# Performance work log

Hardware: AMD Instinct MI355X
Metric: run time of the kernel (lower is better)

Reference implementation:

```python
import jax, jax.numpy as jnp
import numpy as np

V, D, L = 128, 512, 4
B, S = 64, 1024
H = 2 * D          # LSTM hidden size
G = 4 * H          # gate dim (i,f,g,o)
RMS_EPS = 1.1920929e-07  # torch.finfo(float32).eps (nn.RMSNorm default eps=None)
LN_EPS = 1e-5


def setup_inputs() -> dict:
    key = jax.random.key(0)
    ks = jax.random.split(key, 8)
    sc = 1.0 / np.sqrt(H).astype(np.float32)
    return {
        "tokens": jax.random.randint(ks[0], (B, S), 0, V),
        "embedding": jax.random.normal(ks[1], (V, D), jnp.float32) * 0.02,
        "pre_norm_w": jnp.ones((L, D), jnp.float32),
        "W_ih": jax.random.normal(ks[2], (L, G, D), jnp.float32) * sc,
        "W_hh": jax.random.normal(ks[3], (L, G, H), jnp.float32) * sc,
        "b_ih": jnp.zeros((L, G), jnp.float32),
        "b_hh": jnp.zeros((L, G), jnp.float32),
        "W_out": jax.random.normal(ks[4], (L, D, H), jnp.float32) * sc,
        "b_out": jnp.zeros((L, D), jnp.float32),
        "ln_w": jnp.ones((L, D), jnp.float32),
        "ln_b": jnp.zeros((L, D), jnp.float32),
        "final_norm_w": jnp.ones((D,), jnp.float32),
        "head_W": jax.random.normal(ks[5], (V, D), jnp.float32) / np.sqrt(D),
        "head_b": jnp.zeros((V,), jnp.float32),
    }


def rmsnorm(x, w):
    var = jnp.mean(x * x, axis=-1, keepdims=True)
    return x * jax.lax.rsqrt(var + RMS_EPS) * w


def layernorm(x, w, b):
    mu = jnp.mean(x, axis=-1, keepdims=True)
    var = jnp.mean(jnp.square(x - mu), axis=-1, keepdims=True)
    return (x - mu) * jax.lax.rsqrt(var + LN_EPS) * w + b


def lstm(x, W_ih, W_hh, b_ih, b_hh):
    # x: [B,S,D] -> precompute input gates [S,B,4H], scan over time
    xg = jnp.einsum('bsd,gd->sbg', x, W_ih) + b_ih + b_hh
    bsz = x.shape[0]
    hdim = W_hh.shape[1]

    def step(carry, gx):
        h, c = carry
        g = gx + h @ W_hh.T
        i, f, gg, o = jnp.split(g, 4, axis=-1)
        c = jax.nn.sigmoid(f) * c + jax.nn.sigmoid(i) * jnp.tanh(gg)
        h = jax.nn.sigmoid(o) * jnp.tanh(c)
        return (h, c), h

    init = (jnp.zeros((bsz, hdim), x.dtype), jnp.zeros((bsz, hdim), x.dtype))
    _, hs = jax.lax.scan(step, init, xg)
    return hs.transpose(1, 0, 2)  # [B,S,H]


def reference(tokens, embedding, pre_norm_w, W_ih, W_hh, b_ih, b_hh,
              W_out, b_out, ln_w, ln_b, final_norm_w, head_W, head_b):
    x = embedding[tokens]  # [B,S,D]
    n_layers = pre_norm_w.shape[0]
    for l in range(n_layers):
        nx = rmsnorm(x, pre_norm_w[l])
        h = lstm(nx, W_ih[l], W_hh[l], b_ih[l], b_hh[l])
        out = jnp.einsum('bsh,dh->bsd', h, W_out[l]) + b_out[l]
        x = x + layernorm(out + nx, ln_w[l], ln_b[l])
    x = rmsnorm(x, final_norm_w)
    last = x[:, -1, :]                 # last token; dropout is identity (eval)
    return last @ head_W.T + head_b    # [B,V]
```

## Files before the change

kernel.cpp:

```cpp
#include <hip/hip_runtime.h>
#include <stdint.h>

typedef short bf16x8 __attribute__((ext_vector_type(8)));
typedef short s16x4  __attribute__((ext_vector_type(4)));
typedef float f32x4  __attribute__((ext_vector_type(4)));

__device__ __forceinline__ short f2bf(float f) {
  unsigned u = __builtin_bit_cast(unsigned, f);
  unsigned r = (u + 0x7fffu + ((u >> 16) & 1u)) >> 16;
  return (short)r;
}
__device__ __forceinline__ float bf2f(short s) {
  unsigned u = ((unsigned)(unsigned short)s) << 16;
  return __builtin_bit_cast(float, u);
}
__device__ __forceinline__ float sigf(float x) { return 1.f / (1.f + __expf(-x)); }
__device__ __forceinline__ float tanhf_(float x) {
  float e = __expf(2.f * x);
  return 1.f - 2.f / (e + 1.f);
}
__device__ __forceinline__ float wave_sum(float v) {
#pragma unroll
  for (int o = 32; o; o >>= 1) v += __shfl_xor(v, o, 64);
  return v;
}

__global__ void cvt_k(const float* __restrict__ a, short* __restrict__ o, int n) {
  int i = (blockIdx.x * 256 + threadIdx.x) * 4;
  if (i >= n) return;
  float4 v = *(const float4*)(a + i);
  s16x4 r;
  r[0] = f2bf(v.x); r[1] = f2bf(v.y); r[2] = f2bf(v.z); r[3] = f2bf(v.w);
  *(s16x4*)(o + i) = r;
}

__global__ void embed_k(const int* __restrict__ toks, const float* __restrict__ emb,
                        short* __restrict__ x) {
  const int t = blockIdx.x;
  const int tok = toks[t];
  const float4* src = (const float4*)(emb + (size_t)tok * 512);
  float4 a = src[threadIdx.x * 2], b = src[threadIdx.x * 2 + 1];
  bf16x8 o;
  o[0] = f2bf(a.x); o[1] = f2bf(a.y); o[2] = f2bf(a.z); o[3] = f2bf(a.w);
  o[4] = f2bf(b.x); o[5] = f2bf(b.y); o[6] = f2bf(b.z); o[7] = f2bf(b.w);
  *(bf16x8*)(x + (size_t)t * 512 + threadIdx.x * 8) = o;
}

__global__ void rms_k(const short* __restrict__ x, const float* __restrict__ w,
                      short* __restrict__ nx, int s0, int chsh, int chm) {
  const int t = blockIdx.x, b = t >> chsh, sl = t & chm;
  const short* xr = x + ((size_t)b * 1024 + s0 + sl) * 512;
  const int d0 = threadIdx.x * 8;
  bf16x8 xv = *(const bf16x8*)(xr + d0);
  float f[8];
  float ss = 0.f;
#pragma unroll
  for (int i = 0; i < 8; ++i) { f[i] = bf2f(xv[i]); ss += f[i] * f[i]; }
  ss = wave_sum(ss);
  float rs = rsqrtf(ss * (1.f / 512.f) + 1.1920929e-07f);
  float4 w0 = *(const float4*)(w + d0), w1 = *(const float4*)(w + d0 + 4);
  bf16x8 o;
  o[0] = f2bf(f[0] * rs * w0.x); o[1] = f2bf(f[1] * rs * w0.y);
  o[2] = f2bf(f[2] * rs * w0.z); o[3] = f2bf(f[3] * rs * w0.w);
  o[4] = f2bf(f[4] * rs * w1.x); o[5] = f2bf(f[5] * rs * w1.y);
  o[6] = f2bf(f[6] * rs * w1.z); o[7] = f2bf(f[7] * rs * w1.w);
  *(bf16x8*)(nx + (size_t)t * 512 + d0) = o;
}

template <int KD, int MODE>
__global__ __launch_bounds__(256, 2) void gemm_bt_k(
    const short* __restrict__ A, const short* __restrict__ Bw, short* __restrict__ Cb,
    const float* __restrict__ bias0, const float* __restrict__ bias1, int chsh, int chm) {
  __shared__ __align__(16) short lA[128 * 64];
  __shared__ __align__(16) short lB[128 * 64];
  const int tid = threadIdx.x, lane = tid & 63, wv = tid >> 6;
  const int wm = wv >> 1, wn = wv & 1;
  const int tm = blockIdx.x, tn = blockIdx.y;
  f32x4 acc[4][4] = {};
  const short* Abase = A + (size_t)tm * 128 * KD;
  const short* Bbase = Bw + (size_t)tn * 128 * KD;
  for (int k0 = 0; k0 < KD; k0 += 64) {
    __syncthreads();
#pragma unroll
    for (int i = 0; i < 4; ++i) {
      int e = i * 2048 + tid * 8;
      int row = e >> 6, c8 = (e >> 3) & 7;
      int dsto = row * 64 + ((c8 ^ (row & 7)) << 3);
      *(bf16x8*)(lA + dsto) = *(const bf16x8*)(Abase + (size_t)row * KD + k0 + (c8 << 3));
      *(bf16x8*)(lB + dsto) = *(const bf16x8*)(Bbase + (size_t)row * KD + k0 + (c8 << 3));
    }
    __syncthreads();
#pragma unroll
    for (int kk = 0; kk < 2; ++kk) {
      bf16x8 af[4], bfr[4];
#pragma unroll
      for (int i = 0; i < 4; ++i) {
        int ra = wm * 64 + i * 16 + (lane & 15);
        int rb = wn * 64 + i * 16 + (lane & 15);
        int k8 = kk * 4 + (lane >> 4);
        af[i] = *(const bf16x8*)(lA + ra * 64 + ((k8 ^ (ra & 7)) << 3));
        bfr[i] = *(const bf16x8*)(lB + rb * 64 + ((k8 ^ (rb & 7)) << 3));
      }
#pragma unroll
      for (int i = 0; i < 4; ++i)
#pragma unroll
        for (int j = 0; j < 4; ++j)
          acc[i][j] = __builtin_amdgcn_mfma_f32_16x16x32_bf16(af[i], bfr[j], acc[i][j], 0, 0, 0);
    }
  }
#pragma unroll
  for (int i = 0; i < 4; ++i) {
    int rbase = tm * 128 + wm * 64 + i * 16 + (lane >> 4) * 4;
#pragma unroll
    for (int j = 0; j < 4; ++j) {
      int col = tn * 128 + wn * 64 + j * 16 + (lane & 15);
      float badd = 0.f;
      if constexpr (MODE == 0) badd = bias0[col] + bias1[col];
#pragma unroll
      for (int r = 0; r < 4; ++r) {
        int rowi = rbase + r;
        float v = acc[i][j][r] + badd;
        if constexpr (MODE == 0) {
          int b = rowi >> chsh, sl = rowi & chm;
          size_t off = (size_t)sl * 262144 + (size_t)((col >> 4) & 63) * 4096 +
                       (size_t)(b >> 4) * 1024 + (size_t)(col >> 10) * 256 +
                       (size_t)(b & 15) * 16 + (size_t)(col & 15);
          Cb[off] = f2bf(v);
        } else {
          Cb[(size_t)rowi * 512 + col] = f2bf(v);
        }
      }
    }
  }
}

__global__ __launch_bounds__(256, 1) void lstm_rec_k(
    const short* __restrict__ xg,
    short* __restrict__ h_all,
    const short* __restrict__ Whh,
    short* __restrict__ ring,
    float* __restrict__ c_st,
    int CH, int chsh) {
  const int tid = threadIdx.x, lane = tid & 63, wq = tid >> 6;
  const int grp = blockIdx.x >> 6, w = blockIdx.x & 63;
  const int j0 = w * 16, b0 = grp * 16;
  __shared__ __align__(16) short hstg[16384];
  __shared__ float gates[4][16][16];
  bf16x8 wf[32];
  {
    const short* wrow = Whh + (size_t)(wq * 1024 + j0 + (lane & 15)) * 1024 + (lane >> 4) * 8;
#pragma unroll
    for (int kt = 0; kt < 32; ++kt) wf[kt] = *(const bf16x8*)(wrow + kt * 32);
  }
  const int bb = tid >> 3, jj = (tid & 7) * 2;
  float c0 = 0.f, c1 = 0.f;
  if (tid < 128) {
    c0 = c_st[(size_t)(b0 + bb) * 1024 + j0 + jj];
    c1 = c_st[(size_t)(b0 + bb) * 1024 + j0 + jj + 1];
  }
  const short* xgl = xg + (size_t)(w * 4 + grp) * 1024 + wq * 256 +
                     (size_t)(lane & 15) * 16 + (lane >> 4) * 4;
  s16x4 cur = *(const s16x4*)xgl;

  for (int s = 0; s < CH; ++s) {
    const short* slot = ring + (size_t)s * 65536;
    unsigned long long hl0[8], hl1[8];
    unsigned mask = 0;
    while (mask != 0xFFFFu) {
#pragma unroll
      for (int it = 0; it < 8; ++it) {
        int si = it * 256 + tid;
        int kt = si >> 6, sl = si & 63;
        const short* gp = slot + (size_t)(b0 + (sl & 15)) * 1024 + kt * 32 + (sl >> 4) * 8;
        if (!(mask & (1u << (2 * it))))
          hl0[it] = __hip_atomic_load((const unsigned long long*)gp, __ATOMIC_RELAXED,
                                      __HIP_MEMORY_SCOPE_AGENT);
        if (!(mask & (1u << (2 * it + 1))))
          hl1[it] = __hip_atomic_load((const unsigned long long*)(gp + 4), __ATOMIC_RELAXED,
                                      __HIP_MEMORY_SCOPE_AGENT);
      }
      unsigned m = 0;
#pragma unroll
      for (int it = 0; it < 8; ++it) {
        unsigned ok0 = (((unsigned)hl0[it] != 0x7F7F7F7Fu) &
                        ((unsigned)(hl0[it] >> 32) != 0x7F7F7F7Fu)) ? 1u : 0u;
        unsigned ok1 = (((unsigned)hl1[it] != 0x7F7F7F7Fu) &
                        ((unsigned)(hl1[it] >> 32) != 0x7F7F7F7Fu)) ? 1u : 0u;
        m |= (ok0 << (2 * it)) | (ok1 << (2 * it + 1));
      }
      mask = m;
      if (mask != 0xFFFFu) __builtin_amdgcn_s_sleep(1);
    }
#pragma unroll
    for (int it = 0; it < 8; ++it) {
      int si = it * 256 + tid;
      unsigned long long* dst = (unsigned long long*)hstg + (size_t)si * 2;
      dst[0] = hl0[it]; dst[1] = hl1[it];
    }
    __syncthreads();
    f32x4 a0, a1 = {0.f, 0.f, 0.f, 0.f}, a2 = {0.f, 0.f, 0.f, 0.f}, a3 = {0.f, 0.f, 0.f, 0.f};
#pragma unroll
    for (int r = 0; r < 4; ++r) a0[r] = bf2f(cur[r]);
    if (s + 1 < CH) cur = *(const s16x4*)(xgl + (size_t)(s + 1) * 262144);
#pragma unroll
    for (int kt = 0; kt < 32; kt += 4) {
      a0 = __builtin_amdgcn_mfma_f32_16x16x32_bf16(
          wf[kt], *(const bf16x8*)(hstg + kt * 512 + lane * 8), a0, 0, 0, 0);
      a1 = __builtin_amdgcn_mfma_f32_16x16x32_bf16(
          wf[kt + 1], *(const bf16x8*)(hstg + (kt + 1) * 512 + lane * 8), a1, 0, 0, 0);
      a2 = __builtin_amdgcn_mfma_f32_16x16x32_bf16(
          wf[kt + 2], *(const bf16x8*)(hstg + (kt + 2) * 512 + lane * 8), a2, 0, 0, 0);
      a3 = __builtin_amdgcn_mfma_f32_16x16x32_bf16(
          wf[kt + 3], *(const bf16x8*)(hstg + (kt + 3) * 512 + lane * 8), a3, 0, 0, 0);
    }
    f32x4 acc = (a0 + a1) + (a2 + a3);
#pragma unroll
    for (int r = 0; r < 4; ++r) gates[wq][lane & 15][(lane >> 4) * 4 + r] = acc[r];
    __syncthreads();
    if (tid < 128) {
      float i0 = gates[0][bb][jj], i1 = gates[0][bb][jj + 1];
      float f0 = gates[1][bb][jj], f1 = gates[1][bb][jj + 1];
      float g0 = gates[2][bb][jj], g1 = gates[2][bb][jj + 1];
      float o0 = gates[3][bb][jj], o1 = gates[3][bb][jj + 1];
      c0 = sigf(f0) * c0 + sigf(i0) * tanhf_(g0);
      c1 = sigf(f1) * c1 + sigf(i1) * tanhf_(g1);
      float h0 = sigf(o0) * tanhf_(c0);
      float h1 = sigf(o1) * tanhf_(c1);
      unsigned pk = (unsigned)(unsigned short)f2bf(h0) |
                    (((unsigned)(unsigned short)f2bf(h1)) << 16);
      __hip_atomic_store(
          (unsigned*)(ring + (size_t)(s + 1) * 65536 + (size_t)(b0 + bb) * 1024 + j0 + jj),
          pk, __ATOMIC_RELAXED, __HIP_MEMORY_SCOPE_AGENT);
      *(unsigned*)(h_all + ((size_t)(((b0 + bb) << chsh) + s)) * 1024 + j0 + jj) = pk;
    }
  }
  if (tid < 128) {
    c_st[(size_t)(b0 + bb) * 1024 + j0 + jj] = c0;
    c_st[(size_t)(b0 + bb) * 1024 + j0 + jj + 1] = c1;
  }
}

__global__ void ln_k(short* __restrict__ x, const short* __restrict__ outc,
                     const short* __restrict__ nxc, const float* __restrict__ bout,
                     const float* __restrict__ lnw, const float* __restrict__ lnb,
                     int s0, int chsh, int chm) {
  const int t = blockIdx.x, b = t >> chsh, sl = t & chm;
  short* xr = x + ((size_t)b * 1024 + s0 + sl) * 512;
  const int d0 = threadIdx.x * 8;
  bf16x8 ov = *(const bf16x8*)(outc + (size_t)t * 512 + d0);
  bf16x8 nv = *(const bf16x8*)(nxc + (size_t)t * 512 + d0);
  float v[8];
  float s = 0.f, ss = 0.f;
#pragma unroll
  for (int i = 0; i < 8; ++i) {
    v[i] = bf2f(ov[i]) + bout[d0 + i] + bf2f(nv[i]);
    s += v[i]; ss += v[i] * v[i];
  }
  s = wave_sum(s); ss = wave_sum(ss);
  float mu = s * (1.f / 512.f);
  float var = ss * (1.f / 512.f) - mu * mu;
  float rsd = rsqrtf(var + 1e-5f);
  bf16x8 xv = *(const bf16x8*)(xr + d0);
  bf16x8 o;
#pragma unroll
  for (int i = 0; i < 8; ++i)
    o[i] = f2bf(bf2f(xv[i]) + (v[i] - mu) * rsd * lnw[d0 + i] + lnb[d0 + i]);
  *(bf16x8*)(xr + d0) = o;
}

__global__ void head_k(const short* __restrict__ x, const float* __restrict__ fw,
                       const float* __restrict__ hW, const float* __restrict__ hb,
                       float* __restrict__ out) {
  const int b = blockIdx.x, v = threadIdx.x;
  __shared__ float xr[512];
  __shared__ float red[2];
  const short* row = x + ((size_t)b * 1024 + 1023) * 512;
  s16x4 xs = *(const s16x4*)(row + v * 4);
  float x0 = bf2f(xs[0]), x1 = bf2f(xs[1]), x2 = bf2f(xs[2]), x3 = bf2f(xs[3]);
  float ss = x0 * x0 + x1 * x1 + x2 * x2 + x3 * x3;
  ss = wave_sum(ss);
  if ((v & 63) == 0) red[v >> 6] = ss;
  __syncthreads();
  float rs = rsqrtf((red[0] + red[1]) * (1.f / 512.f) + 1.1920929e-07f);
  float4 fwv = *(const float4*)(fw + v * 4);
  xr[v * 4 + 0] = x0 * rs * fwv.x;
  xr[v * 4 + 1] = x1 * rs * fwv.y;
  xr[v * 4 + 2] = x2 * rs * fwv.z;
  xr[v * 4 + 3] = x3 * rs * fwv.w;
  __syncthreads();
  float a = hb[v];
  const float* wr = hW + (size_t)v * 512;
  for (int d = 0; d < 512; d += 4) {
    float4 w4 = *(const float4*)(wr + d);
    a += xr[d] * w4.x + xr[d + 1] * w4.y + xr[d + 2] * w4.z + xr[d + 3] * w4.w;
  }
  out[(size_t)b * 128 + v] = a;
}

extern "C" void kernel_launch(void* const* d_in, const int* in_sizes, int n_in,
                              void* d_out, int out_size, void* d_ws, size_t ws_size,
                              hipStream_t stream) {
  const int* toks = (const int*)d_in[0];
  const float* emb = (const float*)d_in[1];
  const float* prew = (const float*)d_in[2];
  const float* Wih = (const float*)d_in[3];
  const float* Whh = (const float*)d_in[4];
  const float* bih = (const float*)d_in[5];
  const float* bhh = (const float*)d_in[6];
  const float* Wout = (const float*)d_in[7];
  const float* bout = (const float*)d_in[8];
  const float* lnw = (const float*)d_in[9];
  const float* lnb = (const float*)d_in[10];
  const float* fnw = (const float*)d_in[11];
  const float* hW = (const float*)d_in[12];
  const float* hb = (const float*)d_in[13];
  (void)in_sizes; (void)n_in; (void)out_size;

  const size_t fixed = 262144
                     + (size_t)4096 * 512 * 2
                     + (size_t)4096 * 1024 * 2
                     + (size_t)512 * 1024 * 2
                     + (size_t)64 * 1024 * 512 * 2
                     + 131072
                     + 32 * 256;
  int chsh = 5;
  for (int c = 8; c >= 5; --c) {
    size_t per = ((size_t)1 << c) * (65536 + 131072 + 524288 + 131072);
    if (fixed + per <= ws_size) { chsh = c; break; }
  }
  const int CH = 1 << chsh, chm = CH - 1, chunks = 1024 >> chsh;

  char* w = (char*)d_ws;
  size_t off = 0;
  auto alloc = [&](size_t sz) {
    void* p = w + off;
    off = (off + sz + 255) & ~(size_t)255;
    return p;
  };
  float* c_st = (float*)alloc(262144);
  short* ring = (short*)alloc((size_t)(CH + 1) * 131072);
  short* wihb = (short*)alloc((size_t)4096 * 512 * 2);
  short* whhb = (short*)alloc((size_t)4096 * 1024 * 2);
  short* woutb = (short*)alloc((size_t)512 * 1024 * 2);
  short* x = (short*)alloc((size_t)64 * 1024 * 512 * 2);
  short* nx = (short*)alloc((size_t)64 * CH * 512 * 2);
  short* hc = (short*)alloc((size_t)64 * CH * 1024 * 2);
  short* xgb = (short*)alloc((size_t)CH * 64 * 4096 * 2);
  short* outc = xgb;

  embed_k<<<65536, 64, 0, stream>>>(toks, emb, x);

  for (int l = 0; l < 4; ++l) {
    hipMemsetAsync(ring, 0, 131072, stream);
    hipMemsetAsync((char*)ring + 131072, 0x7F, (size_t)CH * 131072, stream);
    hipMemsetAsync(c_st, 0, 262144, stream);
    cvt_k<<<2048, 256, 0, stream>>>(Wih + (size_t)l * 4096 * 512, wihb, 4096 * 512);
    cvt_k<<<4096, 256, 0, stream>>>(Whh + (size_t)l * 4096 * 1024, whhb, 4096 * 1024);
    cvt_k<<<512, 256, 0, stream>>>(Wout + (size_t)l * 512 * 1024, woutb, 512 * 1024);
    for (int ch = 0; ch < chunks; ++ch) {
      const int s0 = ch * CH;
      rms_k<<<64 * CH, 64, 0, stream>>>(x, prew + l * 512, nx, s0, chsh, chm);
      gemm_bt_k<512, 0><<<dim3(CH / 2, 32), 256, 0, stream>>>(
          nx, wihb, xgb, bih + l * 4096, bhh + l * 4096, chsh, chm);
      lstm_rec_k<<<256, 256, 0, stream>>>(xgb, hc, whhb, ring, c_st, CH, chsh);
      if (ch + 1 < chunks) {
        hipMemcpyAsync(ring, (char*)ring + (size_t)CH * 131072, 131072,
                       hipMemcpyDeviceToDevice, stream);
        hipMemsetAsync((char*)ring + 131072, 0x7F, (size_t)CH * 131072, stream);
      }
      gemm_bt_k<1024, 1><<<dim3(CH / 2, 4), 256, 0, stream>>>(
          hc, woutb, outc, nullptr, nullptr, chsh, chm);
      ln_k<<<64 * CH, 64, 0, stream>>>(x, outc, nx, bout + l * 512, lnw + l * 512,
                                       lnb + l * 512, s0, chsh, chm);
    }
  }
  head_k<<<64, 128, 0, stream>>>(x, fnw, hW, hb, (float*)d_out);
}
```

Measured before the change: 24.94 ms.

## Split LSTM recurrent h-polling into halves and prefetch next step's loads

The recurrent kernel now issues the next timestep's h loads before computing the cell update. It then waits only for the first half of h to arrive before starting the MFMAs on that half, and polls the second half during that work, which overlaps cross-block sync latency with compute. The GEMM tile loads now use direct global-to-LDS loads instead of going through registers. The gates LDS array is padded to avoid bank conflicts, and the chunk size search now allows larger chunks (up to 1024 steps), which means fewer kernel launches. The extra polling and barriers add complexity and a risk of stale or early reads.

```diff
diff --git a/kernel.cpp b/kernel.cpp
--- a/kernel.cpp
+++ b/kernel.cpp
@@ -23,6 +23,11 @@
 #pragma unroll
   for (int o = 32; o; o >>= 1) v += __shfl_xor(v, o, 64);
   return v;
+}
+__device__ __forceinline__ void gload_lds16(const short* g, short* l) {
+  __builtin_amdgcn_global_load_lds(
+      (const __attribute__((address_space(1))) unsigned int*)g,
+      (__attribute__((address_space(3))) unsigned int*)l, 16, 0, 0);
 }
 
 __global__ void cvt_k(const float* __restrict__ a, short* __restrict__ o, int n) {
@@ -79,15 +84,15 @@
   f32x4 acc[4][4] = {};
   const short* Abase = A + (size_t)tm * 128 * KD;
   const short* Bbase = Bw + (size_t)tn * 128 * KD;
+  const int row_ = tid >> 3;
+  const int c8s_ = (tid & 7) ^ (row_ & 7);
   for (int k0 = 0; k0 < KD; k0 += 64) {
     __syncthreads();
 #pragma unroll
     for (int i = 0; i < 4; ++i) {
-      int e = i * 2048 + tid * 8;
-      int row = e >> 6, c8 = (e >> 3) & 7;
-      int dsto = row * 64 + ((c8 ^ (row & 7)) << 3);
-      *(bf16x8*)(lA + dsto) = *(const bf16x8*)(Abase + (size_t)row * KD + k0 + (c8 << 3));
-      *(bf16x8*)(lB + dsto) = *(const bf16x8*)(Bbase + (size_t)row * KD + k0 + (c8 << 3));
+      int row = i * 32 + row_;
+      gload_lds16(Abase + (size_t)row * KD + k0 + (c8s_ << 3), lA + i * 2048 + wv * 512);
+      gload_lds16(Bbase + (size_t)row * KD + k0 + (c8s_ << 3), lB + i * 2048 + wv * 512);
     }
     __syncthreads();
 #pragma unroll
@@ -145,7 +150,7 @@
   const int grp = blockIdx.x >> 6, w = blockIdx.x & 63;
   const int j0 = w * 16, b0 = grp * 16;
   __shared__ __align__(16) short hstg[16384];
-  __shared__ float gates[4][16][16];
+  __shared__ float gates[4][16][17];
   bf16x8 wf[32];
   {
     const short* wrow = Whh + (size_t)(wq * 1024 + j0 + (lane & 15)) * 1024 + (lane >> 4) * 8;
@@ -162,48 +167,62 @@
                      (size_t)(lane & 15) * 16 + (lane >> 4) * 4;
   s16x4 cur = *(const s16x4*)xgl;
 
+  unsigned long long hl0[8], hl1[8];
+  unsigned mask = 0;
+
+#define ISSUE(slotp, m)                                                                   \
+  {                                                                                       \
+    _Pragma("unroll") for (int it = 0; it < 8; ++it) {                                    \
+      int si = it * 256 + tid;                                                            \
+      int kt = si >> 6, sl = si & 63;                                                     \
+      const short* gp = (slotp) + (size_t)(b0 + (sl & 15)) * 1024 + kt * 32 + (sl >> 4) * 8; \
+      if (!((m) & (1u << (2 * it))))                                                      \
+        hl0[it] = __hip_atomic_load((const unsigned long long*)gp, __ATOMIC_RELAXED,      \
+                                    __HIP_MEMORY_SCOPE_AGENT);                            \
+      if (!((m) & (1u << (2 * it + 1))))                                                  \
+        hl1[it] = __hip_atomic_load((const unsigned long long*)(gp + 4), __ATOMIC_RELAXED, \
+                                    __HIP_MEMORY_SCOPE_AGENT);                            \
+    }                                                                                     \
+  }
+
+  auto chk = [&](unsigned m) -> unsigned {
+#pragma unroll
+    for (int it = 0; it < 8; ++it) {
+      if (!(m & (1u << (2 * it))) && (unsigned)hl0[it] != 0x7F7F7F7Fu &&
+          (unsigned)(hl0[it] >> 32) != 0x7F7F7F7Fu)
+        m |= 1u << (2 * it);
+      if (!(m & (1u << (2 * it + 1))) && (unsigned)hl1[it] != 0x7F7F7F7Fu &&
+          (unsigned)(hl1[it] >> 32) != 0x7F7F7F7Fu)
+        m |= 1u << (2 * it + 1);
+    }
+    return m;
+  };
+
+  ISSUE(ring, 0u);
+
   for (int s = 0; s < CH; ++s) {
     const short* slot = ring + (size_t)s * 65536;
-    unsigned long long hl0[8], hl1[8];
-    unsigned mask = 0;
-    while (mask != 0xFFFFu) {
-#pragma unroll
-      for (int it = 0; it < 8; ++it) {
-        int si = it * 256 + tid;
-        int kt = si >> 6, sl = si & 63;
-        const short* gp = slot + (size_t)(b0 + (sl & 15)) * 1024 + kt * 32 + (sl >> 4) * 8;
-        if (!(mask & (1u << (2 * it))))
-          hl0[it] = __hip_atomic_load((const unsigned long long*)gp, __ATOMIC_RELAXED,
-                                      __HIP_MEMORY_SCOPE_AGENT);
-        if (!(mask & (1u << (2 * it + 1))))
-          hl1[it] = __hip_atomic_load((const unsigned long long*)(gp + 4), __ATOMIC_RELAXED,
-                                      __HIP_MEMORY_SCOPE_AGENT);
-      }
-      unsigned m = 0;
-#pragma unroll
-      for (int it = 0; it < 8; ++it) {
-        unsigned ok0 = (((unsigned)hl0[it] != 0x7F7F7F7Fu) &
-                        ((unsigned)(hl0[it] >> 32) != 0x7F7F7F7Fu)) ? 1u : 0u;
-        unsigned ok1 = (((unsigned)hl1[it] != 0x7F7F7F7Fu) &
-                        ((unsigned)(hl1[it] >> 32) != 0x7F7F7F7Fu)) ? 1u : 0u;
-        m |= (ok0 << (2 * it)) | (ok1 << (2 * it + 1));
-      }
-      mask = m;
-      if (mask != 0xFFFFu) __builtin_amdgcn_s_sleep(1);
-    }
-#pragma unroll
-    for (int it = 0; it < 8; ++it) {
+    mask = chk(mask);
+    int iter = 0;
+    while ((mask & 0x00FFu) != 0x00FFu) {
+      if (iter++) __builtin_amdgcn_s_sleep(1);
+      ISSUE(slot, mask);
+      mask = chk(mask);
+    }
+#pragma unroll
+    for (int it = 0; it < 4; ++it) {
       int si = it * 256 + tid;
       unsigned long long* dst = (unsigned long long*)hstg + (size_t)si * 2;
       dst[0] = hl0[it]; dst[1] = hl1[it];
     }
     __syncthreads();
+    if ((mask & 0xFF00u) != 0xFF00u) ISSUE(slot, mask | 0x00FFu);
     f32x4 a0, a1 = {0.f, 0.f, 0.f, 0.f}, a2 = {0.f, 0.f, 0.f, 0.f}, a3 = {0.f, 0.f, 0.f, 0.f};
 #pragma unroll
     for (int r = 0; r < 4; ++r) a0[r] = bf2f(cur[r]);
     if (s + 1 < CH) cur = *(const s16x4*)(xgl + (size_t)(s + 1) * 262144);
 #pragma unroll
-    for (int kt = 0; kt < 32; kt += 4) {
+    for (int kt = 0; kt < 16; kt += 4) {
       a0 = __builtin_amdgcn_mfma_f32_16x16x32_bf16(
           wf[kt], *(const bf16x8*)(hstg + kt * 512 + lane * 8), a0, 0, 0, 0);
       a1 = __builtin_amdgcn_mfma_f32_16x16x32_bf16(
@@ -213,10 +232,37 @@
       a3 = __builtin_amdgcn_mfma_f32_16x16x32_bf16(
           wf[kt + 3], *(const bf16x8*)(hstg + (kt + 3) * 512 + lane * 8), a3, 0, 0, 0);
     }
+    mask = chk(mask);
+    iter = 0;
+    while ((mask & 0xFF00u) != 0xFF00u) {
+      if (iter++) __builtin_amdgcn_s_sleep(1);
+      ISSUE(slot, mask);
+      mask = chk(mask);
+    }
+#pragma unroll
+    for (int it = 4; it < 8; ++it) {
+      int si = it * 256 + tid;
+      unsigned long long* dst = (unsigned long long*)hstg + (size_t)si * 2;
+      dst[0] = hl0[it]; dst[1] = hl1[it];
+    }
+    __syncthreads();
+#pragma unroll
+    for (int kt = 16; kt < 32; kt += 4) {
+      a0 = __builtin_amdgcn_mfma_f32_16x16x32_bf16(
+          wf[kt], *(const bf16x8*)(hstg + kt * 512 + lane * 8), a0, 0, 0, 0);
+      a1 = __builtin_amdgcn_mfma_f32_16x16x32_bf16(
+          wf[kt + 1], *(const bf16x8*)(hstg + (kt + 1) * 512 + lane * 8), a1, 0, 0, 0);
+      a2 = __builtin_amdgcn_mfma_f32_16x16x32_bf16(
+          wf[kt + 2], *(const bf16x8*)(hstg + (kt + 2) * 512 + lane * 8), a2, 0, 0, 0);
+      a3 = __builtin_amdgcn_mfma_f32_16x16x32_bf16(
+          wf[kt + 3], *(const bf16x8*)(hstg + (kt + 3) * 512 + lane * 8), a3, 0, 0, 0);
+    }
     f32x4 acc = (a0 + a1) + (a2 + a3);
 #pragma unroll
     for (int r = 0; r < 4; ++r) gates[wq][lane & 15][(lane >> 4) * 4 + r] = acc[r];
     __syncthreads();
+    if (s + 1 < CH) ISSUE(ring + (size_t)(s + 1) * 65536, 0u);
+    mask = 0;
     if (tid < 128) {
       float i0 = gates[0][bb][jj], i1 = gates[0][bb][jj + 1];
       float f0 = gates[1][bb][jj], f1 = gates[1][bb][jj + 1];
@@ -238,6 +284,7 @@
     c_st[(size_t)(b0 + bb) * 1024 + j0 + jj] = c0;
     c_st[(size_t)(b0 + bb) * 1024 + j0 + jj + 1] = c1;
   }
+#undef ISSUE
 }
 
 __global__ void ln_k(short* __restrict__ x, const short* __restrict__ outc,
@@ -324,8 +371,8 @@
                      + 131072
                      + 32 * 256;
   int chsh = 5;
-  for (int c = 8; c >= 5; --c) {
-    size_t per = ((size_t)1 << c) * (65536 + 131072 + 524288 + 131072);
+  for (int c = 10; c >= 5; --c) {
+    size_t per = ((size_t)1 << c) * 851968;
     if (fixed + per <= ws_size) { chsh = c; break; }
   }
   const int CH = 1 << chsh, chm = CH - 1, chunks = 1024 >> chsh;
```

Result: slower. 44.23 ms (+77.4%).
